# Optimization experiments

Hardware: AMD Instinct MI355X
Metric: run time of the kernel (lower is better)

## Reference

```python
import jax, jax.numpy as jnp
import numpy as np

DELTA = 2.5749
BN_EPS = 1e-5
N_LAYERS = 5


def _gin_pna_conv(x, src, dst, nW1, nb1, nW2, nb2, mW, mb):
    # x: [N, D]; src/dst: [E]
    N = x.shape[0]
    msgs = x[src]                                   # [E, D] gather (message = x_j)
    cnt = jax.ops.segment_sum(jnp.ones_like(dst, dtype=x.dtype), dst, num_segments=N)  # [N]
    c = jnp.maximum(cnt, 1.0)[:, None]              # guard isolated nodes
    sums = jax.ops.segment_sum(msgs, dst, num_segments=N)          # [N, D]
    maxs = jax.ops.segment_max(msgs, dst, num_segments=N)
    maxs = jnp.where(cnt[:, None] > 0, maxs, 0.0)   # empty segments -> 0 (torch_scatter behavior)
    means = sums / c
    sq_means = jax.ops.segment_sum(msgs * msgs, dst, num_segments=N) / c
    var = jax.nn.relu(sq_means - means * means)
    base = jnp.concatenate([sums, maxs, means, var], axis=1)        # [N, 4D]
    amp = (c / DELTA) * base                        # amplification scaler
    att = (DELTA / c) * base                        # attenuation scaler
    comb = jnp.concatenate([base, amp, att], axis=1)                # [N, 12D]
    agg = comb @ mW.T + mb                          # mlp: 12D -> D
    h = agg + x                                     # GIN: (1+eps)*x_r + aggr, eps=0
    h = jax.nn.relu(h @ nW1.T + nb1) @ nW2.T + nb2  # nn = Linear-ReLU-Linear
    return h


def _batchnorm(x, gamma, beta):
    mu = jnp.mean(x, axis=0)
    var = jnp.var(x, axis=0)
    return (x - mu) * jax.lax.rsqrt(var + BN_EPS) * gamma + beta


def setup_inputs() -> dict:
    key = jax.random.key(0)
    ks = jax.random.split(key, 12)
    N, E, D, G, OUT = 100000, 1600000, 64, 512, 16
    s = 0.05
    p = lambda k, shape: jax.random.normal(k, shape, dtype=jnp.float32) * s
    return {
        "x": jax.random.normal(ks[0], (N, D), dtype=jnp.float32),
        "edge_index": jax.random.randint(ks[1], (2, E), 0, N),
        "batch": jnp.sort(jax.random.randint(ks[2], (N,), 0, G)),
        "encW": p(ks[3], (D, D)), "encb": jnp.zeros((D,), jnp.float32),
        "nnW1": p(ks[4], (N_LAYERS, D, D)), "nnb1": jnp.zeros((N_LAYERS, D), jnp.float32),
        "nnW2": p(ks[5], (N_LAYERS, D, D)), "nnb2": jnp.zeros((N_LAYERS, D), jnp.float32),
        "mlpW": p(ks[6], (N_LAYERS, D, 12 * D)), "mlpb": jnp.zeros((N_LAYERS, D), jnp.float32),
        "bnG": jnp.ones((N_LAYERS, D), jnp.float32), "bnB": jnp.zeros((N_LAYERS, D), jnp.float32),
        "fc1W": p(ks[7], (D, D)), "fc1b": jnp.zeros((D,), jnp.float32),
        "fc2W": p(ks[8], (OUT, D)), "fc2b": jnp.zeros((OUT,), jnp.float32),
    }


def reference(x, edge_index, batch, encW, encb, nnW1, nnb1, nnW2, nnb2,
              mlpW, mlpb, bnG, bnB, fc1W, fc1b, fc2W, fc2b):
    NUM_GRAPHS = 512
    src, dst = edge_index[0], edge_index[1]
    h = x @ encW.T + encb                           # encoder
    for i in range(N_LAYERS):                       # fixed small layer loop
        h = jax.nn.relu(_gin_pna_conv(h, src, dst, nnW1[i], nnb1[i],
                                      nnW2[i], nnb2[i], mlpW[i], mlpb[i]))
        h = _batchnorm(h, bnG[i], bnB[i])
    g = jax.ops.segment_sum(h, batch, num_segments=NUM_GRAPHS)      # global_add_pool
    g = jax.nn.relu(g @ fc1W.T + fc1b)              # dropout is identity in eval mode
    return g @ fc2W.T + fc2b
```

## Files before the change

### kernel.cpp

```cpp
#include <hip/hip_runtime.h>
#include <hip/hip_bf16.h>
#include <hip/hip_fp16.h>

#define DELTA 2.5749f
#define BN_EPS 1e-5f

#define NBUCK 512
#define NBLK 256
#define ECAP 3584

typedef __attribute__((ext_vector_type(8))) _Float16 f16x8;
typedef __attribute__((ext_vector_type(2))) _Float16 f16x2;
typedef __attribute__((ext_vector_type(4))) float f32x4;

__device__ inline unsigned short f2h(float f) {
    union { _Float16 h; unsigned short u; } v;
    v.h = (_Float16)f;
    return v.u;
}


__global__ __launch_bounds__(512) void k_cnt(const int* __restrict__ dst,
                                             int* __restrict__ cnts,
                                             int E, int npb, int CS) {
    __shared__ int hist[NBUCK];
    int t = threadIdx.x;
    hist[t] = 0;
    __syncthreads();
    int s0 = blockIdx.x * CS, s1 = min(s0 + CS, E);
    for (int e = s0 + t; e < s1; e += 512)
        atomicAdd(&hist[dst[e] / npb], 1);
    __syncthreads();
    cnts[blockIdx.x * NBUCK + t] = hist[t];
}

__global__ void k_bscan1(const int* __restrict__ cnts, int* __restrict__ bases,
                         int* __restrict__ btot) {
    __shared__ int s[NBLK];
    int b = blockIdx.x, t = threadIdx.x;
    int v = cnts[t * NBUCK + b];
    s[t] = v; __syncthreads();
    for (int off = 1; off < NBLK; off <<= 1) {
        int x = (t >= off) ? s[t - off] : 0;
        __syncthreads();
        s[t] += x;
        __syncthreads();
    }
    bases[t * NBUCK + b] = s[t] - v;
    if (t == NBLK - 1) btot[b] = s[t];
}

__global__ void k_btops(const int* __restrict__ btot, int* __restrict__ bbase,
                        int* __restrict__ rowptr, int E, int N) {
    __shared__ int s[NBUCK];
    int t = threadIdx.x;
    int v = btot[t];
    s[t] = v; __syncthreads();
    for (int off = 1; off < NBUCK; off <<= 1) {
        int x = (t >= off) ? s[t - off] : 0;
        __syncthreads();
        s[t] += x;
        __syncthreads();
    }
    bbase[t] = s[t] - v;
    if (t == 0) rowptr[N] = E;
}

__global__ __launch_bounds__(512) void k_scat(const int* __restrict__ dst,
                                              const int* __restrict__ src,
                                              const int* __restrict__ bases,
                                              const int* __restrict__ bbase,
                                              int2* __restrict__ eDS,
                                              int E, int npb, int CS) {
    __shared__ int cur[NBUCK];
    int t = threadIdx.x;
    cur[t] = bbase[t] + bases[blockIdx.x * NBUCK + t];
    __syncthreads();
    int s0 = blockIdx.x * CS, s1 = min(s0 + CS, E);
    for (int e = s0 + t; e < s1; e += 512) {
        int d = dst[e];
        int p = d / npb;
        int pos = atomicAdd(&cur[p], 1);
        eDS[pos] = make_int2(d, src[e]);
    }
}

__global__ __launch_bounds__(256) void k_csr(const int2* __restrict__ eDS,
                                             const int* __restrict__ bbase,
                                             const int* __restrict__ btot,
                                             int* __restrict__ rowptr,
                                             int* __restrict__ col,
                                             float* __restrict__ cnt,
                                             int npb, int N) {
    __shared__ int2 sE[ECAP];
    __shared__ int pre[256], sc[256];
    int b = blockIdx.x, t = threadIdx.x;
    int lo = b * npb;
    if (lo >= N) return;
    int nn = min(npb, N - lo);
    int base = bbase[b], n = btot[b];
    pre[t] = 0;
    __syncthreads();
    const int2* gE = eDS + base;
    for (int i = t; i < n; i += 256) {
        int2 e = gE[i];
        if (i < ECAP) sE[i] = e;
        atomicAdd(&pre[e.x - lo], 1);
    }
    __syncthreads();
    int deg = (t < nn) ? pre[t] : 0;
    sc[t] = deg; __syncthreads();
    for (int off = 1; off < 256; off <<= 1) {
        int x = (t >= off) ? sc[t - off] : 0;
        __syncthreads();
        sc[t] += x;
        __syncthreads();
    }
    int excl = sc[t] - deg;
    if (t < nn) {
        rowptr[lo + t] = base + excl;
        cnt[lo + t] = (float)(deg > 0 ? deg : 1);
    }
    __syncthreads();
    pre[t] = excl;
    __syncthreads();
    for (int i = t; i < n; i += 256) {
        int2 e = (i < ECAP) ? sE[i] : gE[i];
        int pos = atomicAdd(&pre[e.x - lo], 1);
        col[base + pos] = e.y;
    }
}

__global__ void k_castw_mlp(const float* __restrict__ w, unsigned short* __restrict__ o,
                            int total) {
    int i = blockIdx.x * 256 + threadIdx.x;
    if (i >= total) return;
    int lane = i & 63;
    int tile = (i >> 6) % 12;
    int sc = (i / 768) % 8;
    int layer = i / 6144;
    int r16 = lane & 15, quad = lane >> 4;
    int mat = tile >> 2, nt = tile & 3;
    const float* sp = w + (size_t)(layer * 64 + nt * 16 + r16) * 768
                        + mat * 256 + sc * 32 + quad * 8;
    unsigned short* op = o + (size_t)i * 8;
#pragma unroll
    for (int j = 0; j < 8; j++) op[j] = f2h(sp[j]);
}

__global__ void k_castw_nn(const float* __restrict__ w, unsigned short* __restrict__ o,
                           int total) {
    int i = blockIdx.x * 256 + threadIdx.x;
    if (i >= total) return;
    int lane = i & 63;
    int s = (i >> 6) & 1;
    int nt = (i >> 7) & 3;
    int layer = i >> 9;
    int r16 = lane & 15, quad = lane >> 4;
    const float* sp = w + (size_t)(layer * 64 + nt * 16 + r16) * 64 + s * 32 + quad * 8;
    unsigned short* op = o + (size_t)i * 8;
#pragma unroll
    for (int j = 0; j < 8; j++) op[j] = f2h(sp[j]);
}

#define ACC2(V)                                                            \
    do {                                                                   \
        mx = __builtin_elementwise_max(mx, V);                             \
        float x0 = (float)V[0], x1 = (float)V[1];                          \
        sa += x0; qa = fmaf(x0, x0, qa);                                   \
        sb += x1; qb = fmaf(x1, x1, qb);                                   \
    } while (0)

__global__ __launch_bounds__(256) void k_agg(const unsigned short* __restrict__ h16,
                                             const int* __restrict__ rowptr,
                                             const int* __restrict__ col,
                                             const float* __restrict__ bnstat,
                                             const float* __restrict__ gamma,
                                             const float* __restrict__ beta,
                                             float invN, int first,
                                             unsigned short* __restrict__ baseF,
                                             int N) {
    int t = threadIdx.x;
    int lane = t & 63;
    int half = lane >> 5;
    int fl = lane & 31;
    int node = blockIdx.x * 8 + (t >> 6) * 2 + half;
    if (node >= N) return;
    int fo2 = fl * 2;
    float scx, scy, shx, shy;
    if (first) {
        scx = 1.f; scy = 1.f; shx = 0.f; shy = 0.f;
    } else {
        float mu0 = bnstat[fo2] * invN, mu1 = bnstat[fo2 + 1] * invN;
        float v0 = bnstat[64 + fo2] * invN - mu0 * mu0;
        float v1 = bnstat[64 + fo2 + 1] * invN - mu1 * mu1;
        scx = rsqrtf(v0 + BN_EPS) * gamma[fo2];
        scy = rsqrtf(v1 + BN_EPS) * gamma[fo2 + 1];
        shx = beta[fo2] - mu0 * scx;
        shy = beta[fo2 + 1] - mu1 * scy;
    }
    const _Float16* hp = (const _Float16*)h16;
    int s0 = rowptr[node], s1 = rowptr[node + 1];
    int deg = s1 - s0;
    float sa = 0.f, sb = 0.f, qa = 0.f, qb = 0.f;
    f16x2 mx;
    mx[0] = (_Float16)(-65504.0f); mx[1] = (_Float16)(-65504.0f);
    const _Float16* hb = hp + fo2;
    int nfull = deg >> 3;

    f16x2 vA[8];
    int cN[8];
    if (nfull >= 1) {
        int cC[8];
        const int* cp = col + s0;
#pragma unroll
        for (int j = 0; j < 8; j++) cC[j] = cp[j];
        if (nfull >= 2) {
#pragma unroll
            for (int j = 0; j < 8; j++) cN[j] = cp[8 + j];
        }
#pragma unroll
        for (int j = 0; j < 8; j++) vA[j] = *(const f16x2*)(hb + ((size_t)(unsigned)cC[j] << 6));
    }
    for (int b = 1; b < nfull; b++) {
        int cNN[8];
        f16x2 vB[8];
        if (b + 1 < nfull) {
            const int* cp = col + s0 + (b + 1) * 8;
#pragma unroll
            for (int j = 0; j < 8; j++) cNN[j] = cp[j];
        }
#pragma unroll
        for (int j = 0; j < 8; j++) vB[j] = *(const f16x2*)(hb + ((size_t)(unsigned)cN[j] << 6));
#pragma unroll
        for (int j = 0; j < 8; j++) ACC2(vA[j]);
#pragma unroll
        for (int j = 0; j < 8; j++) { vA[j] = vB[j]; }
#pragma unroll
        for (int j = 0; j < 8; j++) { cN[j] = cNN[j]; }
    }
    if (nfull >= 1) {
#pragma unroll
        for (int j = 0; j < 8; j++) ACC2(vA[j]);
    }
    int tb = s0 + nfull * 8;
    int rem = s1 - tb;
    if (rem > 0) {
        int cT[8];
        f16x2 vT[8];
#pragma unroll
        for (int j = 0; j < 8; j++) {
            int idx = (tb + j < s1) ? (tb + j) : (s1 - 1);
            cT[j] = col[idx];
        }
#pragma unroll
        for (int j = 0; j < 8; j++) vT[j] = *(const f16x2*)(hb + ((size_t)(unsigned)cT[j] << 6));
#pragma unroll
        for (int j = 0; j < 8; j++) {
            if (j < rem) ACC2(vT[j]);
        }
    }

    float c = (float)(deg > 0 ? deg : 1);
    float ic = 1.f / c;
    float sum0, sum1, max0, max1, mean0, mean1, var0, var1;
    if (deg == 0) {
        sum0 = sum1 = max0 = max1 = mean0 = mean1 = var0 = var1 = 0.f;
    } else {
        sum0 = fmaf(scx, sa, c * shx);
        sum1 = fmaf(scy, sb, c * shy);
        max0 = fmaf(scx, (float)mx[0], shx);
        max1 = fmaf(scy, (float)mx[1], shy);
        float m0 = sa * ic, m1 = sb * ic;
        mean0 = fmaf(scx, m0, shx);
        mean1 = fmaf(scy, m1, shy);
        var0 = scx * scx * fmaxf(fmaf(-m0, m0, qa * ic), 0.f);
        var1 = scy * scy * fmaxf(fmaf(-m1, m1, qb * ic), 0.f);
    }
    size_t b = (size_t)node * 256 + fo2;
    ushort2 o;
    o.x = f2h(sum0); o.y = f2h(sum1);  *(ushort2*)(baseF + b) = o;
    o.x = f2h(max0); o.y = f2h(max1);  *(ushort2*)(baseF + b + 64) = o;
    o.x = f2h(mean0); o.y = f2h(mean1); *(ushort2*)(baseF + b + 128) = o;
    o.x = f2h(var0); o.y = f2h(var1);  *(ushort2*)(baseF + b + 192) = o;
}

__global__ __launch_bounds__(256) void k_mlp(const unsigned short* __restrict__ baseF,
                                             const float* __restrict__ cnt,
                                             const unsigned short* __restrict__ mW2,
                                             const float* __restrict__ mb,
                                             const unsigned short* __restrict__ hres16,
                                             const float* __restrict__ bnstatPrev,
                                             const float* __restrict__ gammaP,
                                             const float* __restrict__ betaP,
                                             float invN, int first,
                                             const unsigned short* __restrict__ w1F,
                                             const float* __restrict__ b1,
                                             const unsigned short* __restrict__ w2F,
                                             const float* __restrict__ b2,
                                             float* __restrict__ bnstat,
                                             unsigned short* __restrict__ hOut16, int N) {
    __shared__ char smem[36864];
    _Float16* bufA = (_Float16*)smem;
    _Float16* bufB = bufA + 128 * 72;
    _Float16* ldsW = bufB;
    float* red = (float*)bufB;

    int t = threadIdx.x;
    int wave = t >> 6, lane = t & 63;
    int r16 = lane & 15, quad = lane >> 4;
    int n0 = blockIdx.x * 128;
    int m0 = n0 + wave * 32;

    const _Float16* aptr0 = (const _Float16*)baseF + (size_t)(m0 + r16) * 256 + quad * 8;
    const _Float16* aptr1 = aptr0 + 16 * 256;
    f32x4 acc0[12], acc1[12];
#pragma unroll
    for (int i = 0; i < 12; i++) {
        acc0[i] = (f32x4){0.f, 0.f, 0.f, 0.f};
        acc1[i] = (f32x4){0.f, 0.f, 0.f, 0.f};
    }
    uint4 st0, st1, st2;
    {
        const uint4* sp = (const uint4*)mW2;
        st0 = sp[t]; st1 = sp[t + 256]; st2 = sp[t + 512];
    }
    f16x8 aC0 = *(const f16x8*)(aptr0);
    f16x8 aC1 = *(const f16x8*)(aptr1);
    f16x8 aN0 = *(const f16x8*)(aptr0 + 32);
    f16x8 aN1 = *(const f16x8*)(aptr1 + 32);
    {
        uint4* dp = (uint4*)ldsW;
        dp[t] = st0; dp[t + 256] = st1; dp[t + 512] = st2;
    }
    __syncthreads();

#pragma unroll 1
    for (int sc = 0; sc < 8; sc++) {
        if (sc < 7) {
            const uint4* sp = (const uint4*)(mW2 + (sc + 1) * 6144);
            st0 = sp[t]; st1 = sp[t + 256]; st2 = sp[t + 512];
        }
        f16x8 aP0, aP1;
        if (sc < 6) {
            aP0 = *(const f16x8*)(aptr0 + (sc + 2) * 32);
            aP1 = *(const f16x8*)(aptr1 + (sc + 2) * 32);
        }
#pragma unroll
        for (int tile = 0; tile < 12; tile++) {
            f16x8 wF = *(const f16x8*)(ldsW + tile * 512 + lane * 8);
            acc0[tile] = __builtin_amdgcn_mfma_f32_16x16x32_f16(aC0, wF, acc0[tile], 0, 0, 0);
            acc1[tile] = __builtin_amdgcn_mfma_f32_16x16x32_f16(aC1, wF, acc1[tile], 0, 0, 0);
        }
        if (sc < 7) {
            __syncthreads();
            uint4* dp = (uint4*)ldsW;
            dp[t] = st0; dp[t + 256] = st1; dp[t + 512] = st2;
            __syncthreads();
        }
        aC0 = aN0; aC1 = aN1; aN0 = aP0; aN1 = aP1;
    }
    __syncthreads();

    {
        int nl = wave * 32 + (lane >> 1);
        int fo = (lane & 1) * 32;
        int gn = n0 + nl;
        uint4* dp = (uint4*)(bufA + nl * 72 + fo);
        if (gn < N) {
            const uint4* sp = (const uint4*)(hres16 + (size_t)gn * 64 + fo);
            dp[0] = sp[0]; dp[1] = sp[1]; dp[2] = sp[2]; dp[3] = sp[3];
        } else {
            uint4 z = make_uint4(0, 0, 0, 0);
            dp[0] = z; dp[1] = z; dp[2] = z; dp[3] = z;
        }
    }
    __builtin_amdgcn_wave_barrier();

    float scf[4], shf[4], mbv[4];
#pragma unroll
    for (int nt = 0; nt < 4; nt++) {
        int f = nt * 16 + r16;
        mbv[nt] = mb[f];
        if (first) {
            scf[nt] = 1.f; shf[nt] = 0.f;
        } else {
            float mu = bnstatPrev[f] * invN;
            float var = bnstatPrev[64 + f] * invN - mu * mu;
            float s = rsqrtf(var + BN_EPS) * gammaP[f];
            scf[nt] = s; shf[nt] = betaP[f] - mu * s;
        }
    }
#pragma unroll
    for (int mt = 0; mt < 2; mt++) {
#pragma unroll
        for (int i = 0; i < 4; i++) {
            int nl = wave * 32 + mt * 16 + quad * 4 + i;
            int gn = n0 + nl;
            if (gn < N) {
                float c = cnt[gn];
                float amp = c / DELTA, att = DELTA / c;
                f32x4* a = mt ? acc1 : acc0;
#pragma unroll
                for (int nt = 0; nt < 4; nt++) {
                    int f = nt * 16 + r16;
                    float r = (float)bufA[nl * 72 + f];
                    float v = a[nt][i] + amp * a[4 + nt][i] + att * a[8 + nt][i]
                            + mbv[nt] + fmaf(r, scf[nt], shf[nt]);
                    bufA[nl * 72 + f] = (_Float16)v;
                }
            }
        }
    }
    __builtin_amdgcn_wave_barrier();

    f32x4 accN[8];
#pragma unroll
    for (int i = 0; i < 8; i++) accN[i] = (f32x4){0.f, 0.f, 0.f, 0.f};
#pragma unroll
    for (int s = 0; s < 2; s++) {
        f16x8 fA0 = *(const f16x8*)(bufA + (wave * 32 + r16) * 72 + s * 32 + quad * 8);
        f16x8 fA1 = *(const f16x8*)(bufA + (wave * 32 + 16 + r16) * 72 + s * 32 + quad * 8);
#pragma unroll
        for (int nt = 0; nt < 4; nt++) {
            f16x8 wB = *(const f16x8*)((const _Float16*)w1F + ((nt * 2 + s) * 64 + lane) * 8);
            accN[nt]     = __builtin_amdgcn_mfma_f32_16x16x32_f16(fA0, wB, accN[nt], 0, 0, 0);
            accN[4 + nt] = __builtin_amdgcn_mfma_f32_16x16x32_f16(fA1, wB, accN[4 + nt], 0, 0, 0);
        }
    }
    float b1v[4];
#pragma unroll
    for (int nt = 0; nt < 4; nt++) b1v[nt] = b1[nt * 16 + r16];
#pragma unroll
    for (int mt = 0; mt < 2; mt++) {
#pragma unroll
        for (int i = 0; i < 4; i++) {
            int nl = wave * 32 + mt * 16 + quad * 4 + i;
#pragma unroll
            for (int nt = 0; nt < 4; nt++) {
                float v = fmaxf(accN[mt * 4 + nt][i] + b1v[nt], 0.f);
                bufB[nl * 72 + nt * 16 + r16] = (_Float16)v;
            }
        }
    }
    __builtin_amdgcn_wave_barrier();

    f32x4 accM[8];
#pragma unroll
    for (int i = 0; i < 8; i++) accM[i] = (f32x4){0.f, 0.f, 0.f, 0.f};
#pragma unroll
    for (int s = 0; s < 2; s++) {
        f16x8 fA0 = *(const f16x8*)(bufB + (wave * 32 + r16) * 72 + s * 32 + quad * 8);
        f16x8 fA1 = *(const f16x8*)(bufB + (wave * 32 + 16 + r16) * 72 + s * 32 + quad * 8);
#pragma unroll
        for (int nt = 0; nt < 4; nt++) {
            f16x8 wB = *(const f16x8*)((const _Float16*)w2F + ((nt * 2 + s) * 64 + lane) * 8);
            accM[nt]     = __builtin_amdgcn_mfma_f32_16x16x32_f16(fA0, wB, accM[nt], 0, 0, 0);
            accM[4 + nt] = __builtin_amdgcn_mfma_f32_16x16x32_f16(fA1, wB, accM[4 + nt], 0, 0, 0);
        }
    }
    float b2v[4], s1[4], s2[4];
#pragma unroll
    for (int nt = 0; nt < 4; nt++) {
        b2v[nt] = b2[nt * 16 + r16]; s1[nt] = 0.f; s2[nt] = 0.f;
    }
#pragma unroll
    for (int mt = 0; mt < 2; mt++) {
#pragma unroll
        for (int i = 0; i < 4; i++) {
            int nl = wave * 32 + mt * 16 + quad * 4 + i;
            bool ok = (n0 + nl) < N;
#pragma unroll
            for (int nt = 0; nt < 4; nt++) {
                float v = fmaxf(accM[mt * 4 + nt][i] + b2v[nt], 0.f);
                if (ok) { s1[nt] += v; s2[nt] = fmaf(v, v, s2[nt]); }
                bufA[nl * 72 + nt * 16 + r16] = (_Float16)v;
            }
        }
    }
    __builtin_amdgcn_wave_barrier();

    {
        int nl = wave * 32 + (lane >> 1);
        int fo = (lane & 1) * 32;
        int gn = n0 + nl;
        if (gn < N) {
            const uint4* sp = (const uint4*)(bufA + nl * 72 + fo);
            uint4* dp = (uint4*)(hOut16 + (size_t)gn * 64 + fo);
            dp[0] = sp[0]; dp[1] = sp[1]; dp[2] = sp[2]; dp[3] = sp[3];
        }
    }

    __syncthreads();
#pragma unroll
    for (int nt = 0; nt < 4; nt++) {
        int row = wave * 4 + quad;
        red[row * 64 + nt * 16 + r16] = s1[nt];
        red[1024 + row * 64 + nt * 16 + r16] = s2[nt];
    }
    __syncthreads();
    if (t < 128) {
        int d = t & 63, part = t >> 6;
        float tot = 0.f;
#pragma unroll
        for (int r = 0; r < 16; r++) tot += red[part * 1024 + r * 64 + d];
        atomicAdd(&bnstat[part * 64 + d], tot);
    }
}

#define FMA16(ACC0, ACC1, ACC2, ACC3, A, W)                                \
    do {                                                                   \
        ACC0.x = fmaf(A.x, W.x, ACC0.x); ACC0.y = fmaf(A.x, W.y, ACC0.y);  \
        ACC0.z = fmaf(A.x, W.z, ACC0.z); ACC0.w = fmaf(A.x, W.w, ACC0.w);  \
        ACC1.x = fmaf(A.y, W.x, ACC1.x); ACC1.y = fmaf(A.y, W.y, ACC1.y);  \
        ACC1.z = fmaf(A.y, W.z, ACC1.z); ACC1.w = fmaf(A.y, W.w, ACC1.w);  \
        ACC2.x = fmaf(A.z, W.x, ACC2.x); ACC2.y = fmaf(A.z, W.y, ACC2.y);  \
        ACC2.z = fmaf(A.z, W.z, ACC2.z); ACC2.w = fmaf(A.z, W.w, ACC2.w);  \
        ACC3.x = fmaf(A.w, W.x, ACC3.x); ACC3.y = fmaf(A.w, W.y, ACC3.y);  \
        ACC3.z = fmaf(A.w, W.z, ACC3.z); ACC3.w = fmaf(A.w, W.w, ACC3.w);  \
    } while (0)

__global__ __launch_bounds__(256) void k_gemm64(const float* __restrict__ in,
                                                const float* __restrict__ W,
                                                const float* __restrict__ bias,
                                                unsigned short* __restrict__ out16, int N) {
    __shared__ float sInT[64][64];
    __shared__ float sWT[64][64];
    int t = threadIdx.x;
    int tx = t & 15, ty = t >> 4;
    int n0 = blockIdx.x * 64;
    int c4 = tx * 4;
#pragma unroll
    for (int ch = 0; ch < 4; ch++) {
        int row = ch * 16 + ty;
        float4 v = make_float4(0.f, 0.f, 0.f, 0.f);
        if (n0 + row < N) v = *(const float4*)(in + (size_t)(n0 + row) * 64 + c4);
        sInT[c4 + 0][row] = v.x; sInT[c4 + 1][row] = v.y;
        sInT[c4 + 2][row] = v.z; sInT[c4 + 3][row] = v.w;
        float4 w = *(const float4*)(W + (size_t)row * 64 + c4);
        sWT[c4 + 0][row] = w.x; sWT[c4 + 1][row] = w.y;
        sWT[c4 + 2][row] = w.z; sWT[c4 + 3][row] = w.w;
    }
    __syncthreads();
    float4 acc0 = make_float4(0.f, 0.f, 0.f, 0.f);
    float4 acc1 = acc0, acc2 = acc0, acc3 = acc0;
#pragma unroll 8
    for (int k = 0; k < 64; k++) {
        float4 a = *(const float4*)(&sInT[k][ty * 4]);
        float4 w = *(const float4*)(&sWT[k][tx * 4]);
        FMA16(acc0, acc1, acc2, acc3, a, w);
    }
    float4 b4 = *(const float4*)(bias + tx * 4);
#pragma unroll
    for (int i = 0; i < 4; i++) {
        int n = n0 + ty * 4 + i;
        if (n < N) {
            float4 v = (i == 0) ? acc0 : (i == 1) ? acc1 : (i == 2) ? acc2 : acc3;
            v.x += b4.x; v.y += b4.y; v.z += b4.z; v.w += b4.w;
            ushort4 o;
            o.x = f2h(v.x); o.y = f2h(v.y); o.z = f2h(v.z); o.w = f2h(v.w);
            *(ushort4*)(out16 + (size_t)n * 64 + tx * 4) = o;
        }
    }
}

__global__ void k_pool(const unsigned short* __restrict__ h16, const int* __restrict__ batch,
                       const float* __restrict__ bnstat, const float* __restrict__ gamma,
                       const float* __restrict__ beta, float invN,
                       float* __restrict__ g, int N) {
    int d = threadIdx.x & 63, r = threadIdx.x >> 6;
    float mu = bnstat[d] * invN;
    float var = bnstat[64 + d] * invN - mu * mu;
    float sc = rsqrtf(var + BN_EPS) * gamma[d];
    float sh = beta[d] - mu * sc;
    const _Float16* hp = (const _Float16*)h16;
    int nbase = blockIdx.x * 32;
    float acc = 0.f;
    int gcur = -1;
    for (int i = 0; i < 8; i++) {
        int n = nbase + i * 4 + r;
        if (n < N) {
            int gb = batch[n];
            if (gb != gcur) {
                if (gcur >= 0) atomicAdd(&g[gcur * 64 + d], acc);
                acc = 0.f; gcur = gb;
            }
            acc += fmaf((float)hp[(size_t)n * 64 + d], sc, sh);
        }
    }
    if (gcur >= 0) atomicAdd(&g[gcur * 64 + d], acc);
}

__global__ void k_head(const float* __restrict__ g, const float* __restrict__ fc1W,
                       const float* __restrict__ fc1b, const float* __restrict__ fc2W,
                       const float* __restrict__ fc2b, float* __restrict__ out) {
    __shared__ float sg[64], sg1[64];
    int gi = blockIdx.x, t = threadIdx.x;
    sg[t] = g[gi * 64 + t];
    __syncthreads();
    float a = fc1b[t];
    for (int k = 0; k < 64; k++) a = fmaf(sg[k], fc1W[t * 64 + k], a);
    sg1[t] = fmaxf(a, 0.f);
    __syncthreads();
    if (t < 16) {
        float o = fc2b[t];
        for (int k = 0; k < 64; k++) o = fmaf(sg1[k], fc2W[t * 64 + k], o);
        out[gi * 16 + t] = o;
    }
}

extern "C" void kernel_launch(void* const* d_in, const int* in_sizes, int n_in,
                              void* d_out, int out_size, void* d_ws, size_t ws_size,
                              hipStream_t stream) {
    const float* x       = (const float*)d_in[0];
    const int*   eidx    = (const int*)d_in[1];
    const int*   batch   = (const int*)d_in[2];
    const float* encW    = (const float*)d_in[3];
    const float* encb    = (const float*)d_in[4];
    const float* nnW1    = (const float*)d_in[5];
    const float* nnb1    = (const float*)d_in[6];
    const float* nnW2    = (const float*)d_in[7];
    const float* nnb2    = (const float*)d_in[8];
    const float* mlpW    = (const float*)d_in[9];
    const float* mlpb    = (const float*)d_in[10];
    const float* bnG     = (const float*)d_in[11];
    const float* bnB     = (const float*)d_in[12];
    const float* fc1W    = (const float*)d_in[13];
    const float* fc1b    = (const float*)d_in[14];
    const float* fc2W    = (const float*)d_in[15];
    const float* fc2b    = (const float*)d_in[16];
    float* out = (float*)d_out;

    const int N = in_sizes[0] / 64;
    const int E = in_sizes[1] / 2;
    const int G = 512;
    const int* src = eidx;
    const int* dst = eidx + E;
    const int npb = (N + NBUCK - 1) / NBUCK;
    const float invN = 1.f / (float)N;
    const int CS = (E + NBLK - 1) / NBLK;

    char* ws = (char*)d_ws;
    size_t off = 0;
    auto alloc = [&](size_t bytes) { size_t r = off; off = (off + bytes + 255) & ~(size_t)255; return r; };
    int*   rowptr  = (int*)(ws + alloc((size_t)(N + 1) * 4));
    int*   col     = (int*)(ws + alloc((size_t)E * 4));
    int2*  eDS     = (int2*)(ws + alloc((size_t)E * 8));
    int*   cnts    = (int*)(ws + alloc((size_t)NBLK * NBUCK * 4));
    int*   bases   = (int*)(ws + alloc((size_t)NBLK * NBUCK * 4));
    int*   btot    = (int*)(ws + alloc(NBUCK * 4));
    int*   bbase   = (int*)(ws + alloc(NBUCK * 4));
    float* cnt     = (float*)(ws + alloc((size_t)N * 4));
    unsigned short* baseF = (unsigned short*)(ws + alloc((size_t)N * 256 * 2 + 131072));
    unsigned short* hC16 = (unsigned short*)(ws + alloc((size_t)N * 64 * 2 + 32768));
    unsigned short* mWF  = (unsigned short*)(ws + alloc((size_t)5 * 64 * 768 * 2));
    unsigned short* nW1F = (unsigned short*)(ws + alloc((size_t)5 * 64 * 64 * 2));
    unsigned short* nW2F = (unsigned short*)(ws + alloc((size_t)5 * 64 * 64 * 2));
    float* bnstats = (float*)(ws + alloc(5 * 128 * 4));
    float* gpool   = (float*)(ws + alloc((size_t)G * 64 * 4));

    hipMemsetAsync(bnstats, 0, 5 * 128 * 4, stream);
    hipMemsetAsync(gpool, 0, (size_t)G * 64 * 4, stream);

    int ngrid64 = (N + 63) / 64;
    int ngrid128 = (N + 127) / 128;

    k_cnt<<<NBLK, 512, 0, stream>>>(dst, cnts, E, npb, CS);
    k_bscan1<<<NBUCK, NBLK, 0, stream>>>(cnts, bases, btot);
    k_btops<<<1, NBUCK, 0, stream>>>(btot, bbase, rowptr, E, N);
    k_scat<<<NBLK, 512, 0, stream>>>(dst, src, bases, bbase, eDS, E, npb, CS);
    k_csr<<<NBUCK, 256, 0, stream>>>(eDS, bbase, btot, rowptr, col, cnt, npb, N);

    k_castw_mlp<<<120, 256, 0, stream>>>(mlpW, mWF, 30720);
    k_castw_nn<<<10, 256, 0, stream>>>(nnW1, nW1F, 2560);
    k_castw_nn<<<10, 256, 0, stream>>>(nnW2, nW2F, 2560);

    k_gemm64<<<ngrid64, 256, 0, stream>>>(x, encW, encb, hC16, N);

    for (int i = 0; i < 5; i++) {
        const float* bsPrev = (i == 0) ? bnstats : bnstats + (i - 1) * 128;
        const float* gP = (i == 0) ? bnG : bnG + (i - 1) * 64;
        const float* bP = (i == 0) ? bnB : bnB + (i - 1) * 64;
        int first = (i == 0) ? 1 : 0;
        k_agg<<<(N + 7) / 8, 256, 0, stream>>>(hC16, rowptr, col, bsPrev, gP, bP,
                                               invN, first, baseF, N);
        k_mlp<<<ngrid128, 256, 0, stream>>>(baseF, cnt,
                                            mWF + (size_t)i * 49152, mlpb + i * 64,
                                            hC16, bsPrev, gP, bP, invN, first,
                                            nW1F + (size_t)i * 4096, nnb1 + i * 64,
                                            nW2F + (size_t)i * 4096, nnb2 + i * 64,
                                            bnstats + i * 128, hC16, N);
    }

    k_pool<<<(N + 31) / 32, 256, 0, stream>>>(hC16, batch, bnstats + 4 * 128,
                                              bnG + 4 * 64, bnB + 4 * 64, invN, gpool, N);
    k_head<<<G, 64, 0, stream>>>(gpool, fc1W, fc1b, fc2W, fc2b, out);
}
```

Baseline: 627.2 us.

## Fuse neighbor aggregation into MLP kernel with ping-pong node feature buffers

Removes the separate aggregation kernel and does the gather-based sum/max/mean/var aggregation at the start of the MLP kernel. Each wave handles its own 32 rows in 16 passes before the GEMM stages, which saves one launch per layer. Because the gather now runs in the same kernel that writes the new features, node features ping-pong between two buffers to avoid read/write races. The trade-off is less parallelism for the irregular gather: 4 waves per 128 nodes instead of one wave per 2 nodes. The aggregated features still round-trip through global memory in baseF.

Measured after the change: 838.6 us. +33.7%, slower.

```diff
diff --git a/kernel.cpp b/kernel.cpp
--- a/kernel.cpp
+++ b/kernel.cpp
@@ -171,121 +171,9 @@
         sb += x1; qb = fmaf(x1, x1, qb);                                   \
     } while (0)
 
-__global__ __launch_bounds__(256) void k_agg(const unsigned short* __restrict__ h16,
-                                             const int* __restrict__ rowptr,
+__global__ __launch_bounds__(256) void k_mlp(const int* __restrict__ rowptr,
                                              const int* __restrict__ col,
-                                             const float* __restrict__ bnstat,
-                                             const float* __restrict__ gamma,
-                                             const float* __restrict__ beta,
-                                             float invN, int first,
                                              unsigned short* __restrict__ baseF,
-                                             int N) {
-    int t = threadIdx.x;
-    int lane = t & 63;
-    int half = lane >> 5;
-    int fl = lane & 31;
-    int node = blockIdx.x * 8 + (t >> 6) * 2 + half;
-    if (node >= N) return;
-    int fo2 = fl * 2;
-    float scx, scy, shx, shy;
-    if (first) {
-        scx = 1.f; scy = 1.f; shx = 0.f; shy = 0.f;
-    } else {
-        float mu0 = bnstat[fo2] * invN, mu1 = bnstat[fo2 + 1] * invN;
-        float v0 = bnstat[64 + fo2] * invN - mu0 * mu0;
-        float v1 = bnstat[64 + fo2 + 1] * invN - mu1 * mu1;
-        scx = rsqrtf(v0 + BN_EPS) * gamma[fo2];
-        scy = rsqrtf(v1 + BN_EPS) * gamma[fo2 + 1];
-        shx = beta[fo2] - mu0 * scx;
-        shy = beta[fo2 + 1] - mu1 * scy;
-    }
-    const _Float16* hp = (const _Float16*)h16;
-    int s0 = rowptr[node], s1 = rowptr[node + 1];
-    int deg = s1 - s0;
-    float sa = 0.f, sb = 0.f, qa = 0.f, qb = 0.f;
-    f16x2 mx;
-    mx[0] = (_Float16)(-65504.0f); mx[1] = (_Float16)(-65504.0f);
-    const _Float16* hb = hp + fo2;
-    int nfull = deg >> 3;
-
-    f16x2 vA[8];
-    int cN[8];
-    if (nfull >= 1) {
-        int cC[8];
-        const int* cp = col + s0;
-#pragma unroll
-        for (int j = 0; j < 8; j++) cC[j] = cp[j];
-        if (nfull >= 2) {
-#pragma unroll
-            for (int j = 0; j < 8; j++) cN[j] = cp[8 + j];
-        }
-#pragma unroll
-        for (int j = 0; j < 8; j++) vA[j] = *(const f16x2*)(hb + ((size_t)(unsigned)cC[j] << 6));
-    }
-    for (int b = 1; b < nfull; b++) {
-        int cNN[8];
-        f16x2 vB[8];
-        if (b + 1 < nfull) {
-            const int* cp = col + s0 + (b + 1) * 8;
-#pragma unroll
-            for (int j = 0; j < 8; j++) cNN[j] = cp[j];
-        }
-#pragma unroll
-        for (int j = 0; j < 8; j++) vB[j] = *(const f16x2*)(hb + ((size_t)(unsigned)cN[j] << 6));
-#pragma unroll
-        for (int j = 0; j < 8; j++) ACC2(vA[j]);
-#pragma unroll
-        for (int j = 0; j < 8; j++) { vA[j] = vB[j]; }
-#pragma unroll
-        for (int j = 0; j < 8; j++) { cN[j] = cNN[j]; }
-    }
-    if (nfull >= 1) {
-#pragma unroll
-        for (int j = 0; j < 8; j++) ACC2(vA[j]);
-    }
-    int tb = s0 + nfull * 8;
-    int rem = s1 - tb;
-    if (rem > 0) {
-        int cT[8];
-        f16x2 vT[8];
-#pragma unroll
-        for (int j = 0; j < 8; j++) {
-            int idx = (tb + j < s1) ? (tb + j) : (s1 - 1);
-            cT[j] = col[idx];
-        }
-#pragma unroll
-        for (int j = 0; j < 8; j++) vT[j] = *(const f16x2*)(hb + ((size_t)(unsigned)cT[j] << 6));
-#pragma unroll
-        for (int j = 0; j < 8; j++) {
-            if (j < rem) ACC2(vT[j]);
-        }
-    }
-
-    float c = (float)(deg > 0 ? deg : 1);
-    float ic = 1.f / c;
-    float sum0, sum1, max0, max1, mean0, mean1, var0, var1;
-    if (deg == 0) {
-        sum0 = sum1 = max0 = max1 = mean0 = mean1 = var0 = var1 = 0.f;
-    } else {
-        sum0 = fmaf(scx, sa, c * shx);
-        sum1 = fmaf(scy, sb, c * shy);
-        max0 = fmaf(scx, (float)mx[0], shx);
-        max1 = fmaf(scy, (float)mx[1], shy);
-        float m0 = sa * ic, m1 = sb * ic;
-        mean0 = fmaf(scx, m0, shx);
-        mean1 = fmaf(scy, m1, shy);
-        var0 = scx * scx * fmaxf(fmaf(-m0, m0, qa * ic), 0.f);
-        var1 = scy * scy * fmaxf(fmaf(-m1, m1, qb * ic), 0.f);
-    }
-    size_t b = (size_t)node * 256 + fo2;
-    ushort2 o;
-    o.x = f2h(sum0); o.y = f2h(sum1);  *(ushort2*)(baseF + b) = o;
-    o.x = f2h(max0); o.y = f2h(max1);  *(ushort2*)(baseF + b + 64) = o;
-    o.x = f2h(mean0); o.y = f2h(mean1); *(ushort2*)(baseF + b + 128) = o;
-    o.x = f2h(var0); o.y = f2h(var1);  *(ushort2*)(baseF + b + 192) = o;
-}
-
-__global__ __launch_bounds__(256) void k_mlp(const unsigned short* __restrict__ baseF,
                                              const float* __restrict__ cnt,
                                              const unsigned short* __restrict__ mW2,
                                              const float* __restrict__ mb,
@@ -311,6 +199,115 @@
     int r16 = lane & 15, quad = lane >> 4;
     int n0 = blockIdx.x * 128;
     int m0 = n0 + wave * 32;
+
+    {
+        int half = lane >> 5;
+        int fl = lane & 31;
+        int fo2 = fl * 2;
+        float scx, scy, shx, shy;
+        if (first) {
+            scx = 1.f; scy = 1.f; shx = 0.f; shy = 0.f;
+        } else {
+            float mu0 = bnstatPrev[fo2] * invN, mu1 = bnstatPrev[fo2 + 1] * invN;
+            float v0 = bnstatPrev[64 + fo2] * invN - mu0 * mu0;
+            float v1 = bnstatPrev[64 + fo2 + 1] * invN - mu1 * mu1;
+            scx = rsqrtf(v0 + BN_EPS) * gammaP[fo2];
+            scy = rsqrtf(v1 + BN_EPS) * gammaP[fo2 + 1];
+            shx = betaP[fo2] - mu0 * scx;
+            shy = betaP[fo2 + 1] - mu1 * scy;
+        }
+        const _Float16* hp = (const _Float16*)hres16;
+        const _Float16* hb = hp + fo2;
+#pragma unroll 1
+        for (int pass = 0; pass < 16; ++pass) {
+            int node = m0 + pass * 2 + half;
+            if (node >= N) continue;
+            int s0 = rowptr[node], s1 = rowptr[node + 1];
+            int deg = s1 - s0;
+            float sa = 0.f, sb = 0.f, qa = 0.f, qb = 0.f;
+            f16x2 mx;
+            mx[0] = (_Float16)(-65504.0f); mx[1] = (_Float16)(-65504.0f);
+            int nfull = deg >> 3;
+            f16x2 vA[8];
+            int cN[8];
+            if (nfull >= 1) {
+                int cC[8];
+                const int* cp = col + s0;
+#pragma unroll
+                for (int j = 0; j < 8; j++) cC[j] = cp[j];
+                if (nfull >= 2) {
+#pragma unroll
+                    for (int j = 0; j < 8; j++) cN[j] = cp[8 + j];
+                }
+#pragma unroll
+                for (int j = 0; j < 8; j++)
+                    vA[j] = *(const f16x2*)(hb + ((size_t)(unsigned)cC[j] << 6));
+            }
+            for (int b = 1; b < nfull; b++) {
+                int cNN[8];
+                f16x2 vB[8];
+                if (b + 1 < nfull) {
+                    const int* cp = col + s0 + (b + 1) * 8;
+#pragma unroll
+                    for (int j = 0; j < 8; j++) cNN[j] = cp[j];
+                }
+#pragma unroll
+                for (int j = 0; j < 8; j++)
+                    vB[j] = *(const f16x2*)(hb + ((size_t)(unsigned)cN[j] << 6));
+#pragma unroll
+                for (int j = 0; j < 8; j++) ACC2(vA[j]);
+#pragma unroll
+                for (int j = 0; j < 8; j++) { vA[j] = vB[j]; }
+#pragma unroll
+                for (int j = 0; j < 8; j++) { cN[j] = cNN[j]; }
+            }
+            if (nfull >= 1) {
+#pragma unroll
+                for (int j = 0; j < 8; j++) ACC2(vA[j]);
+            }
+            int tb = s0 + nfull * 8;
+            int rem = s1 - tb;
+            if (rem > 0) {
+                int cT[8];
+                f16x2 vT[8];
+#pragma unroll
+                for (int j = 0; j < 8; j++) {
+                    int idx = (tb + j < s1) ? (tb + j) : (s1 - 1);
+                    cT[j] = col[idx];
+                }
+#pragma unroll
+                for (int j = 0; j < 8; j++)
+                    vT[j] = *(const f16x2*)(hb + ((size_t)(unsigned)cT[j] << 6));
+#pragma unroll
+                for (int j = 0; j < 8; j++) {
+                    if (j < rem) ACC2(vT[j]);
+                }
+            }
+            float c = (float)(deg > 0 ? deg : 1);
+            float ic = 1.f / c;
+            float sum0, sum1, max0, max1, mean0, mean1, var0, var1;
+            if (deg == 0) {
+                sum0 = sum1 = max0 = max1 = mean0 = mean1 = var0 = var1 = 0.f;
+            } else {
+                sum0 = fmaf(scx, sa, c * shx);
+                sum1 = fmaf(scy, sb, c * shy);
+                max0 = fmaf(scx, (float)mx[0], shx);
+                max1 = fmaf(scy, (float)mx[1], shy);
+                float m0f = sa * ic, m1f = sb * ic;
+                mean0 = fmaf(scx, m0f, shx);
+                mean1 = fmaf(scy, m1f, shy);
+                var0 = scx * scx * fmaxf(fmaf(-m0f, m0f, qa * ic), 0.f);
+                var1 = scy * scy * fmaxf(fmaf(-m1f, m1f, qb * ic), 0.f);
+            }
+            size_t bo = (size_t)node * 256 + fo2;
+            ushort2 o;
+            o.x = f2h(sum0); o.y = f2h(sum1);  *(ushort2*)(baseF + bo) = o;
+            o.x = f2h(max0); o.y = f2h(max1);  *(ushort2*)(baseF + bo + 64) = o;
+            o.x = f2h(mean0); o.y = f2h(mean1); *(ushort2*)(baseF + bo + 128) = o;
+            o.x = f2h(var0); o.y = f2h(var1);  *(ushort2*)(baseF + bo + 192) = o;
+        }
+    }
+    __syncthreads();
 
     const _Float16* aptr0 = (const _Float16*)baseF + (size_t)(m0 + r16) * 256 + quad * 8;
     const _Float16* aptr1 = aptr0 + 16 * 256;
@@ -652,7 +649,8 @@
     int*   bbase   = (int*)(ws + alloc(NBUCK * 4));
     float* cnt     = (float*)(ws + alloc((size_t)N * 4));
     unsigned short* baseF = (unsigned short*)(ws + alloc((size_t)N * 256 * 2 + 131072));
-    unsigned short* hC16 = (unsigned short*)(ws + alloc((size_t)N * 64 * 2 + 32768));
+    unsigned short* hA   = (unsigned short*)(ws + alloc((size_t)N * 64 * 2 + 32768));
+    unsigned short* hB   = (unsigned short*)(ws + alloc((size_t)N * 64 * 2 + 32768));
     unsigned short* mWF  = (unsigned short*)(ws + alloc((size_t)5 * 64 * 768 * 2));
     unsigned short* nW1F = (unsigned short*)(ws + alloc((size_t)5 * 64 * 64 * 2));
     unsigned short* nW2F = (unsigned short*)(ws + alloc((size_t)5 * 64 * 64 * 2));
@@ -675,24 +673,24 @@
     k_castw_nn<<<10, 256, 0, stream>>>(nnW1, nW1F, 2560);
     k_castw_nn<<<10, 256, 0, stream>>>(nnW2, nW2F, 2560);
 
-    k_gemm64<<<ngrid64, 256, 0, stream>>>(x, encW, encb, hC16, N);
+    k_gemm64<<<ngrid64, 256, 0, stream>>>(x, encW, encb, hA, N);
 
     for (int i = 0; i < 5; i++) {
         const float* bsPrev = (i == 0) ? bnstats : bnstats + (i - 1) * 128;
         const float* gP = (i == 0) ? bnG : bnG + (i - 1) * 64;
         const float* bP = (i == 0) ? bnB : bnB + (i - 1) * 64;
         int first = (i == 0) ? 1 : 0;
-        k_agg<<<(N + 7) / 8, 256, 0, stream>>>(hC16, rowptr, col, bsPrev, gP, bP,
-                                               invN, first, baseF, N);
-        k_mlp<<<ngrid128, 256, 0, stream>>>(baseF, cnt,
+        unsigned short* hIn  = (i & 1) ? hB : hA;
+        unsigned short* hOut = (i & 1) ? hA : hB;
+        k_mlp<<<ngrid128, 256, 0, stream>>>(rowptr, col, baseF, cnt,
                                             mWF + (size_t)i * 49152, mlpb + i * 64,
-                                            hC16, bsPrev, gP, bP, invN, first,
+                                            hIn, bsPrev, gP, bP, invN, first,
                                             nW1F + (size_t)i * 4096, nnb1 + i * 64,
                                             nW2F + (size_t)i * 4096, nnb2 + i * 64,
-                                            bnstats + i * 128, hC16, N);
-    }
-
-    k_pool<<<(N + 31) / 32, 256, 0, stream>>>(hC16, batch, bnstats + 4 * 128,
+                                            bnstats + i * 128, hOut, N);
+    }
+
+    k_pool<<<(N + 31) / 32, 256, 0, stream>>>(hB, batch, bnstats + 4 * 128,
                                               bnG + 4 * 64, bnB + 4 * 64, invN, gpool, N);
     k_head<<<G, 64, 0, stream>>>(gpool, fc1W, fc1b, fc2W, fc2b, out);
 }
```
